# Kernel optimization log

Measured on AMD Instinct MI355X. Metric: run time of the kernel, lower is better.

## Reference

```python
import jax, jax.numpy as jnp
import numpy as np

B, T, D = 4, 512, 512
NB, NH, PF, K = 2, 8, 2, 4
INNER = PF * D          # 1024
DH = INNER // NH        # 128
NC = 1000
EPS = 1e-5


def _ln(x, s, b):
    mu = x.mean(-1, keepdims=True)
    var = x.var(-1, keepdims=True)
    return (x - mu) / jnp.sqrt(var + EPS) * s + b


def _causal_conv(x, k, b):
    # x: [B,T,C], depthwise kernel k: [C,K]
    kk = k.shape[-1]
    xp = jnp.pad(x, ((0, 0), (kk - 1, 0), (0, 0)))
    t = x.shape[1]
    y = sum(xp[:, j:j + t, :] * k[:, j] for j in range(kk))
    return y + b


def _mlstm_scan(q, k, v, ip, fp):
    # q,k,v: [B,T,NH,DH]; ip,fp: [B,T,NH]
    b, t, nh, dh = q.shape
    C0 = jnp.zeros((b, nh, dh, dh), q.dtype)
    n0 = jnp.zeros((b, nh, dh), q.dtype)
    m0 = jnp.zeros((b, nh), q.dtype)

    def step(carry, xs):
        C, n, m = carry
        qt, kt, vt, ipt, fpt = xs
        fl = jax.nn.log_sigmoid(fpt)
        m_new = jnp.maximum(fl + m, ipt)
        i = jnp.exp(ipt - m_new)
        f = jnp.exp(fl + m - m_new)
        C = f[..., None, None] * C + i[..., None, None] * (vt[..., :, None] * kt[..., None, :])
        n = f[..., None] * n + i[..., None] * kt
        denom = jnp.maximum(jnp.abs(jnp.einsum('bhd,bhd->bh', n, qt)), 1.0)
        h = jnp.einsum('bhij,bhj->bhi', C, qt) / denom[..., None]
        return (C, n, m_new), h

    tm = lambda a: jnp.swapaxes(a, 0, 1)  # time-major
    _, h = jax.lax.scan(step, (C0, n0, m0), (tm(q), tm(k), tm(v), tm(ip), tm(fp)))
    return jnp.swapaxes(h, 0, 1)  # [B,T,NH,DH]


def _block(x, ln_s, ln_b, w_up, b_up, conv_k, conv_b, w_q, w_k, w_v,
           w_ig, b_ig, w_fg, b_fg, hn_s, w_down, b_down):
    b, t, d = x.shape
    xn = _ln(x, ln_s, ln_b)
    up = xn @ w_up + b_up                       # [B,T,2*INNER]
    xu, z = up[..., :INNER], up[..., INNER:]
    xc = jax.nn.silu(_causal_conv(xu, conv_k, conv_b))
    q = (xc @ w_q).reshape(b, t, NH, DH)
    k = (xc @ w_k).reshape(b, t, NH, DH) * (DH ** -0.5)
    v = (xu @ w_v).reshape(b, t, NH, DH)
    ip = xc @ w_ig + b_ig                       # [B,T,NH]
    fp = xc @ w_fg + b_fg
    h = _mlstm_scan(q, k, v, ip, fp)            # [B,T,NH,DH]
    mu = h.mean(-1, keepdims=True)
    var = h.var(-1, keepdims=True)
    h = (h - mu) / jnp.sqrt(var + EPS) * hn_s   # per-head norm, hn_s: [NH,DH]
    h = h.reshape(b, t, INNER) * jax.nn.silu(z)
    return x + h @ w_down + b_down


def setup_inputs() -> dict:
    key = jax.random.key(0)
    ks = jax.random.split(key, 24)
    g = lambda i, sh, sc: jax.random.normal(ks[i], sh, jnp.float32) * sc
    inp = {
        'x': g(0, (B, T, D), 1.0),
        'cls_token': g(1, (1, 1, D), 0.02),
        'ln_s': jnp.ones((NB, D)), 'ln_b': jnp.zeros((NB, D)),
        'w_up': g(2, (NB, D, 2 * INNER), D ** -0.5), 'b_up': jnp.zeros((NB, 2 * INNER)),
        'conv_k': g(3, (NB, INNER, K), 0.3), 'conv_b': jnp.zeros((NB, INNER)),
        'w_q': g(4, (NB, INNER, INNER), INNER ** -0.5),
        'w_k': g(5, (NB, INNER, INNER), INNER ** -0.5),
        'w_v': g(6, (NB, INNER, INNER), INNER ** -0.5),
        'w_ig': g(7, (NB, INNER, NH), INNER ** -0.5), 'b_ig': jnp.zeros((NB, NH)),
        'w_fg': g(8, (NB, INNER, NH), INNER ** -0.5),
        'b_fg': jnp.full((NB, NH), 3.0),
        'hn_s': jnp.ones((NB, NH, DH)),
        'w_down': g(9, (NB, INNER, D), INNER ** -0.5), 'b_down': jnp.zeros((NB, D)),
        'fc_ln_s': jnp.ones((D,)), 'fc_ln_b': jnp.zeros((D,)),
        'fc_w': g(10, (D, NC), D ** -0.5), 'fc_b': jnp.zeros((NC,)),
    }
    return inp


def reference(x, cls_token, ln_s, ln_b, w_up, b_up, conv_k, conv_b, w_q, w_k, w_v,
              w_ig, b_ig, w_fg, b_fg, hn_s, w_down, b_down,
              fc_ln_s, fc_ln_b, fc_w, fc_b):
    b = x.shape[0]
    # append class token at the last position ('last')
    h = jnp.concatenate([x, jnp.broadcast_to(cls_token, (b, 1, x.shape[-1]))], axis=1)
    for i in range(NB):
        h = _block(h, ln_s[i], ln_b[i], w_up[i], b_up[i], conv_k[i], conv_b[i],
                   w_q[i], w_k[i], w_v[i], w_ig[i], b_ig[i], w_fg[i], b_fg[i],
                   hn_s[i], w_down[i], b_down[i])
    cls = h[:, -1, :]
    y = jax.nn.relu(_ln(cls, fc_ln_s, fc_ln_b)) @ fc_w + fc_b
    return y
```

## Files before the change

kernel.cpp:

```cpp
#include <hip/hip_runtime.h>

#define EPSV 1e-5f
constexpr int Bsz = 4, T0 = 512, Dm = 512, NHh = 8, KK = 4;
constexpr int TT = 513;
constexpr int IN = 1024, DHd = 128, NCc = 1000;
constexpr int ROWS = Bsz * TT;
constexpr int MPAD = 2176;
constexpr int NCH = 9;

constexpr size_t WT_UP = 0;
constexpr size_t WT_Q  = WT_UP + 2048 * 512;
constexpr size_t WT_K  = WT_Q + 1024 * 1024;
constexpr size_t WT_V  = WT_K + 1024 * 1024;
constexpr size_t WT_DN = WT_V + 1024 * 1024;
constexpr size_t WT_STRIDE = WT_DN + 512 * 1024;

typedef __attribute__((ext_vector_type(8))) short bf16x8;
typedef __attribute__((ext_vector_type(4))) float f32x4;
typedef __attribute__((ext_vector_type(4))) unsigned short ushort4v;
typedef __attribute__((ext_vector_type(8))) unsigned short ushort8v;
typedef unsigned short u16;

__device__ __forceinline__ float siluf(float x) { return x / (1.f + __expf(-x)); }
__device__ __forceinline__ u16 f2bf(float f) {
    unsigned int u = __float_as_uint(f);
    u = (u + 0x7FFFu + ((u >> 16) & 1u)) >> 16;
    return (u16)u;
}
__device__ __forceinline__ float bfu(u16 u) {
    return __uint_as_float(((unsigned int)u) << 16);
}
__device__ __forceinline__ void gload16(const u16* g, u16* l) {
    __builtin_amdgcn_global_load_lds(
        (const __attribute__((address_space(1))) void*)g,
        (__attribute__((address_space(3))) void*)l, 16, 0, 0);
}

template<bool CAT>
__global__ __launch_bounds__(256) void ln_kernel(const float* __restrict__ in,
                                                 const float* __restrict__ x,
                                                 const float* __restrict__ cls,
                                                 const float* __restrict__ s,
                                                 const float* __restrict__ bb,
                                                 float* __restrict__ hout,
                                                 u16* __restrict__ out16) {
    int row = blockIdx.x, tid = threadIdx.x;
    float x0, x1;
    if (CAT) {
        int b = row / TT, t = row - b * TT;
        const float* src = (t < T0) ? (x + ((size_t)(b * T0 + t)) * Dm) : cls;
        x0 = src[tid]; x1 = src[tid + 256];
        hout[(size_t)row * Dm + tid] = x0;
        hout[(size_t)row * Dm + tid + 256] = x1;
    } else {
        const float* r = in + (size_t)row * Dm;
        x0 = r[tid]; x1 = r[tid + 256];
    }
    __shared__ float s1[4], s2[4];
    float sum = x0 + x1, sq = x0 * x0 + x1 * x1;
#pragma unroll
    for (int o = 32; o > 0; o >>= 1) { sum += __shfl_xor(sum, o); sq += __shfl_xor(sq, o); }
    if ((tid & 63) == 0) { s1[tid >> 6] = sum; s2[tid >> 6] = sq; }
    __syncthreads();
    sum = s1[0] + s1[1] + s1[2] + s1[3];
    sq  = s2[0] + s2[1] + s2[2] + s2[3];
    float mu = sum / Dm, var = sq / Dm - mu * mu, inv = rsqrtf(var + EPSV);
    out16[(size_t)row * Dm + tid]       = f2bf((x0 - mu) * inv * s[tid] + bb[tid]);
    out16[(size_t)row * Dm + tid + 256] = f2bf((x1 - mu) * inv * s[tid + 256] + bb[tid + 256]);
}

__global__ __launch_bounds__(256) void w_transpose_kernel(const float* __restrict__ wup,
        const float* __restrict__ wq, const float* __restrict__ wk,
        const float* __restrict__ wv, const float* __restrict__ wdn,
        const float* __restrict__ wig, const float* __restrict__ wfg,
        u16* __restrict__ wt, float* __restrict__ gwt) {
    int y = blockIdx.y;
    if (y >= 10) {
        int blk = y - 10;
        int idx = blockIdx.x * 256 + threadIdx.x;
        if (idx < 16 * IN) {
            int k = idx & 1023;
            int g = (idx >> 10) & 15;
            const float* w = (g < 8) ? (wig + (size_t)blk * IN * NHh)
                                     : (wfg + (size_t)blk * IN * NHh);
            gwt[(size_t)blk * 16 * IN + idx] = w[k * NHh + (g & 7)];
        }
        return;
    }
    int blk = y / 5, sel = y - blk * 5;
    int Kd, N; const float* src; size_t doff;
    if (sel == 0)      { Kd = 512;  N = 2048; src = wup + (size_t)blk * 512 * 2048; doff = WT_UP; }
    else if (sel == 1) { Kd = 1024; N = 1024; src = wq  + (size_t)blk * 1024 * 1024; doff = WT_Q; }
    else if (sel == 2) { Kd = 1024; N = 1024; src = wk  + (size_t)blk * 1024 * 1024; doff = WT_K; }
    else if (sel == 3) { Kd = 1024; N = 1024; src = wv  + (size_t)blk * 1024 * 1024; doff = WT_V; }
    else               { Kd = 1024; N = 512;  src = wdn + (size_t)blk * 1024 * 512;  doff = WT_DN; }
    u16* dst = wt + (size_t)blk * WT_STRIDE + doff;
    int ntx = N >> 5;
    int ntiles = ntx * (Kd >> 5);
    int ti = blockIdx.x;
    if (ti >= ntiles) return;
    int tk = ti / ntx, tn = ti - tk * ntx;
    __shared__ u16 s[32][33];
    int tx = threadIdx.x & 31, ty = threadIdx.x >> 5;
#pragma unroll
    for (int i = 0; i < 4; i++) {
        int k = tk * 32 + ty + i * 8;
        s[ty + i * 8][tx] = f2bf(src[(size_t)k * N + tn * 32 + tx]);
    }
    __syncthreads();
#pragma unroll
    for (int i = 0; i < 4; i++) {
        int n = tn * 32 + ty + i * 8;
        dst[(size_t)n * Kd + tk * 32 + tx] = s[tx][ty + i * 8];
    }
}

template<int BM, int BN>
__device__ __forceinline__ void gemm_tile_body(const u16* __restrict__ A, int lda,
                                               const u16* __restrict__ Wt, int Kd,
                                               const float* __restrict__ bias,
                                               const float* __restrict__ resid, int ldr,
                                               float* __restrict__ Cout, int ldc,
                                               int M, float scale, int m0, int n0,
                                               u16 (*As)[BM][40], u16 (*Bs)[BN][40]) {
    constexpr int MT = BM / 32;
    constexpr int NT = BN / 32;
    constexpr int ANV = BM / 64;
    constexpr int BNV = BN / 64;
    int tid = threadIdx.x;
    int wave = tid >> 6, lane = tid & 63;
    int wm = (wave >> 1) * (BM / 2), wn = (wave & 1) * (BN / 2);
    int lrow = lane & 15, lquad = lane >> 4;

    f32x4 acc[MT][NT];
#pragma unroll
    for (int i = 0; i < MT; i++)
#pragma unroll
        for (int j = 0; j < NT; j++)
#pragma unroll
            for (int r = 0; r < 4; r++) acc[i][j][r] = 0.f;

    int am, ak, bn, bk;
    if (BM == 128) { am = tid >> 1; ak = (tid & 1) * 16; }
    else           { am = tid >> 2; ak = (tid & 3) * 8; }
    if (BN == 128) { bn = tid & 127; bk = (tid >> 7) * 16; }
    else           { bn = tid & 63;  bk = (tid >> 6) * 8; }
    int gm = m0 + am;
    const u16* arow = A + (size_t)(gm < M ? gm : 0) * lda + ak;
    bool avalid = gm < M;
    const u16* wrow = Wt + (size_t)(n0 + bn) * Kd + bk;

    ushort8v areg[ANV];
    ushort8v breg[BNV];

    auto load_tile = [&](int k0) {
        if (avalid) {
#pragma unroll
            for (int i = 0; i < ANV; i++) areg[i] = *(const ushort8v*)(arow + k0 + i * 8);
        } else {
#pragma unroll
            for (int i = 0; i < ANV; i++) areg[i] = (ushort8v){0,0,0,0,0,0,0,0};
        }
#pragma unroll
        for (int i = 0; i < BNV; i++) breg[i] = *(const ushort8v*)(wrow + k0 + i * 8);
    };
    auto store_tile = [&](int buf) {
#pragma unroll
        for (int i = 0; i < ANV; i++)
            *(ushort8v*)&As[buf][am][ak + i * 8] = areg[i];
#pragma unroll
        for (int i = 0; i < BNV; i++)
            *(ushort8v*)&Bs[buf][bn][bk + i * 8] = breg[i];
    };

    load_tile(0);
    store_tile(0);
    __syncthreads();

    int nk = Kd >> 5;
#pragma unroll 1
    for (int it = 0; it < nk; it++) {
        int cur = it & 1;
        bool more = (it + 1 < nk);
        if (more) load_tile((it + 1) << 5);
        bf16x8 afr[MT], bfr[NT];
#pragma unroll
        for (int mt = 0; mt < MT; mt++)
            afr[mt] = *(const bf16x8*)&As[cur][wm + mt * 16 + lrow][lquad * 8];
#pragma unroll
        for (int nt = 0; nt < NT; nt++)
            bfr[nt] = *(const bf16x8*)&Bs[cur][wn + nt * 16 + lrow][lquad * 8];
#pragma unroll
        for (int mt = 0; mt < MT; mt++)
#pragma unroll
            for (int nt = 0; nt < NT; nt++)
                acc[mt][nt] = __builtin_amdgcn_mfma_f32_16x16x32_bf16(
                    afr[mt], bfr[nt], acc[mt][nt], 0, 0, 0);
        if (more) store_tile(cur ^ 1);
        __syncthreads();
    }

#pragma unroll
    for (int mt = 0; mt < MT; mt++) {
#pragma unroll
        for (int r = 0; r < 4; r++) {
            int gmr = m0 + wm + mt * 16 + lquad * 4 + r;
            if (gmr >= M) continue;
#pragma unroll
            for (int nt = 0; nt < NT; nt++) {
                int gn = n0 + wn + nt * 16 + lrow;
                float v = acc[mt][nt][r] * scale;
                if (bias) v += bias[gn];
                if (resid) v += resid[(size_t)gmr * ldr + gn];
                Cout[(size_t)gmr * ldc + gn] = v;
            }
        }
    }
}

template<int BM, int BN>
__global__ __launch_bounds__(256, 2) void gemm_mfma_kernel(const u16* __restrict__ A, int lda,
                                                           const u16* __restrict__ Wt, int Kd,
                                                           const float* __restrict__ bias,
                                                           const float* __restrict__ resid, int ldr,
                                                           float* __restrict__ Cout, int ldc,
                                                           int M, float scale) {
    __shared__ __align__(16) u16 As[2][BM][40];
    __shared__ __align__(16) u16 Bs[2][BN][40];
    gemm_tile_body<BM, BN>(A, lda, Wt, Kd, bias, resid, ldr, Cout, ldc, M, scale,
                           blockIdx.y * BM, blockIdx.x * BN, As, Bs);
}

template<bool OUT16>
__device__ __forceinline__ void gemm128_body(const u16* __restrict__ A, int lda,
                                             const u16* __restrict__ Wt, int Kd,
                                             const float* __restrict__ bias,
                                             void* __restrict__ Cout, int ldc,
                                             int M, float scale, int m0, int n0,
                                             u16* As, u16* Bs) {
    int tid = threadIdx.x;
    int wave = tid >> 6, lane = tid & 63;
    int lrow = lane & 15, lquad = lane >> 4;
    int wm = (wave >> 1) * 64, wn = (wave & 1) * 64;

    const u16* ag0 = A + (size_t)(m0 + wave * 16 + (lane >> 2)) * lda + (lane & 3) * 8;
    const u16* ag1 = ag0 + (size_t)64 * lda;
    const u16* bg0 = Wt + (size_t)(n0 + wave * 16 + (lane >> 2)) * Kd + (lane & 3) * 8;
    const u16* bg1 = bg0 + (size_t)64 * Kd;

    auto stage = [&](int buf, int k0) {
        u16* a = As + buf * 4096 + wave * 512;
        u16* bb = Bs + buf * 4096 + wave * 512;
        gload16(ag0 + k0, a);
        gload16(ag1 + k0, a + 2048);
        gload16(bg0 + k0, bb);
        gload16(bg1 + k0, bb + 2048);
    };

    f32x4 acc[4][4];
#pragma unroll
    for (int i = 0; i < 4; i++)
#pragma unroll
        for (int j = 0; j < 4; j++)
#pragma unroll
            for (int r = 0; r < 4; r++) acc[i][j][r] = 0.f;

    int nk = Kd >> 5;
    stage(0, 0);
    __syncthreads();
#pragma unroll 1
    for (int it = 0; it < nk; it++) {
        int cur = it & 1;
        if (it + 1 < nk) stage(cur ^ 1, (it + 1) << 5);
        const u16* Ac = As + cur * 4096;
        const u16* Bc = Bs + cur * 4096;
        bf16x8 afr[4], bfr[4];
#pragma unroll
        for (int mt = 0; mt < 4; mt++)
            afr[mt] = *(const bf16x8*)&Ac[(wm + mt * 16 + lrow) * 32 + lquad * 8];
#pragma unroll
        for (int nt = 0; nt < 4; nt++)
            bfr[nt] = *(const bf16x8*)&Bc[(wn + nt * 16 + lrow) * 32 + lquad * 8];
#pragma unroll
        for (int mt = 0; mt < 4; mt++)
#pragma unroll
            for (int nt = 0; nt < 4; nt++)
                acc[mt][nt] = __builtin_amdgcn_mfma_f32_16x16x32_bf16(
                    afr[mt], bfr[nt], acc[mt][nt], 0, 0, 0);
        __syncthreads();
    }

#pragma unroll
    for (int mt = 0; mt < 4; mt++) {
#pragma unroll
        for (int r = 0; r < 4; r++) {
            int gmr = m0 + wm + mt * 16 + lquad * 4 + r;
            if (gmr >= M) continue;
#pragma unroll
            for (int nt = 0; nt < 4; nt++) {
                int gn = n0 + wn + nt * 16 + lrow;
                float v = acc[mt][nt][r] * scale;
                if (bias) v += bias[gn];
                if (OUT16) ((u16*)Cout)[(size_t)gmr * ldc + gn] = f2bf(v);
                else       ((float*)Cout)[(size_t)gmr * ldc + gn] = v;
            }
        }
    }
}

__global__ __launch_bounds__(256, 2) void up_gl_kernel(const u16* __restrict__ A,
        const u16* __restrict__ Wt, const float* __restrict__ bias, float* __restrict__ C) {
    __shared__ __align__(16) u16 As[2 * 4096];
    __shared__ __align__(16) u16 Bs[2 * 4096];
    gemm128_body<false>(A, Dm, Wt, Dm, bias, C, 2 * IN, ROWS, 1.f,
                        blockIdx.y * 128, blockIdx.x * 128, As, Bs);
}

__global__ __launch_bounds__(256, 2) void qkv_gl_kernel(const u16* __restrict__ xc16,
                                                        const u16* __restrict__ xu16,
                                                        const u16* __restrict__ wtblk,
                                                        u16* __restrict__ fq,
                                                        u16* __restrict__ fk,
                                                        u16* __restrict__ fv,
                                                        float kscale) {
    __shared__ __align__(16) u16 As[2 * 4096];
    __shared__ __align__(16) u16 Bs[2 * 4096];
    int sel = blockIdx.x >> 3, nx = blockIdx.x & 7;
    const u16* A = (sel == 2) ? xu16 : xc16;
    const u16* Wt = wtblk + ((sel == 0) ? WT_Q : (sel == 1) ? WT_K : WT_V);
    u16* C = (sel == 0) ? fq : (sel == 1) ? fk : fv;
    float scale = (sel == 1) ? kscale : 1.f;
    gemm128_body<true>(A, IN, Wt, IN, nullptr, C, IN, ROWS, scale,
                       blockIdx.y * 128, nx * 128, As, Bs);
}

__global__ __launch_bounds__(256) void convgates_kernel(const float* __restrict__ up,
        const float* __restrict__ ck, const float* __restrict__ cb,
        const float* __restrict__ wt, const float* __restrict__ big,
        const float* __restrict__ bfg,
        u16* __restrict__ xc16, u16* __restrict__ xu16,
        float* __restrict__ ip, float* __restrict__ fp) {
    int row = blockIdx.x, tid = threadIdx.x;
    int b = row / TT, t = row - b * TT;
    __shared__ float sx[IN];
    int c0 = tid * 4;
    float4 cur = *(const float4*)(up + (size_t)row * (2 * IN) + c0);
    float a0 = cb[c0 + 0] + cur.x * ck[(c0 + 0) * KK + 3];
    float a1 = cb[c0 + 1] + cur.y * ck[(c0 + 1) * KK + 3];
    float a2 = cb[c0 + 2] + cur.z * ck[(c0 + 2) * KK + 3];
    float a3 = cb[c0 + 3] + cur.w * ck[(c0 + 3) * KK + 3];
#pragma unroll
    for (int j = 0; j < KK - 1; j++) {
        int tt2 = t - (KK - 1) + j;
        if (tt2 >= 0) {
            float4 pv = *(const float4*)(up + ((size_t)(b * TT + tt2)) * (2 * IN) + c0);
            a0 += pv.x * ck[(c0 + 0) * KK + j];
            a1 += pv.y * ck[(c0 + 1) * KK + j];
            a2 += pv.z * ck[(c0 + 2) * KK + j];
            a3 += pv.w * ck[(c0 + 3) * KK + j];
        }
    }
    float s0 = siluf(a0), s1v = siluf(a1), s2v = siluf(a2), s3v = siluf(a3);
    *(float4*)&sx[c0] = make_float4(s0, s1v, s2v, s3v);
    ushort4v xc4 = {f2bf(s0), f2bf(s1v), f2bf(s2v), f2bf(s3v)};
    *(ushort4v*)&xc16[(size_t)row * IN + c0] = xc4;
    ushort4v xu4 = {f2bf(cur.x), f2bf(cur.y), f2bf(cur.z), f2bf(cur.w)};
    *(ushort4v*)&xu16[(size_t)row * IN + c0] = xu4;
    __syncthreads();

    int g = tid >> 4, l = tid & 15;
    const float* wrow = wt + g * IN;
    float acc = 0.f;
#pragma unroll
    for (int j = 0; j < 16; j++) {
        int k = j * 64 + l * 4;
        float4 w4 = *(const float4*)(wrow + k);
        float4 x4 = *(const float4*)&sx[k];
        acc += w4.x * x4.x + w4.y * x4.y + w4.z * x4.z + w4.w * x4.w;
    }
#pragma unroll
    for (int o = 8; o > 0; o >>= 1) acc += __shfl_down(acc, o, 16);
    if (l == 0) {
        if (g < 8) ip[(size_t)row * NHh + g] = acc + big[g];
        else       fp[(size_t)row * NHh + (g - 8)] = acc + bfg[g - 8];
    }
}

__global__ __launch_bounds__(256, 2) void chunk_state_kernel(const u16* __restrict__ kk,
        const u16* __restrict__ vv, const float* __restrict__ ip,
        const float* __restrict__ fp, float* __restrict__ gG, float* __restrict__ gM,
        float* __restrict__ gMb, float* __restrict__ gDec,
        u16* __restrict__ P16, float* __restrict__ nP) {
    int c = blockIdx.x, chain = blockIdx.y;
    int b = chain >> 3, h = chain & 7;
    int t0 = c * 64;
    int nvalid = min(64, TT - t0);
    __shared__ __align__(16) u16 sWv[128][72];
    __shared__ __align__(16) u16 sKt[128][72];
    __shared__ float sw[64];
    __shared__ float sGf[TT];
    __shared__ float sMbl[NCH];
    int tid = threadIdx.x;

    if (tid < 64) {
        constexpr int PER = 9;
        int lane = tid;
        int tbase = lane * PER;
        float lcs[PER], gi[PER];
        float csum = 0.f;
#pragma unroll
        for (int i = 0; i < PER; i++) {
            int t = tbase + i;
            float fpv = 0.f, ipv = 0.f;
            if (t < TT) {
                size_t gidx = (size_t)(b * TT + t) * NHh + h;
                fpv = fp[gidx]; ipv = ip[gidx];
            }
            float flv = (fpv >= 0.f) ? -log1pf(__expf(-fpv)) : (fpv - log1pf(__expf(fpv)));
            if (t >= TT) flv = 0.f;
            csum += flv;
            lcs[i] = csum;
            gi[i] = ipv;
        }
        float ps = csum;
#pragma unroll
        for (int o = 1; o < 64; o <<= 1) {
            float v = __shfl_up(ps, o);
            if (lane >= o) ps += v;
        }
        float Fexcl = ps - csum;
        float G[PER];
        float cmax = -1e30f;
#pragma unroll
        for (int i = 0; i < PER; i++) {
            int t = tbase + i;
            G[i] = (t < TT) ? (gi[i] - (Fexcl + lcs[i])) : -1e30f;
            cmax = fmaxf(cmax, G[i]);
            lcs[i] = cmax;
        }
        float pm = cmax;
#pragma unroll
        for (int o = 1; o < 64; o <<= 1) {
            float v = __shfl_up(pm, o);
            if (lane >= o) pm = fmaxf(pm, v);
        }
        float Me = __shfl_up(pm, 1);
        if (lane == 0) Me = -1e30f;
#pragma unroll
        for (int i = 0; i < PER; i++) {
            int t = tbase + i;
            if (t < TT) {
                float Mt = fmaxf(0.f, fmaxf(Me, lcs[i]));
                sGf[t] = G[i];
                if (c == 0) { gG[chain * TT + t] = G[i]; gM[chain * TT + t] = Mt; }
                if (((t & 63) == 63) || t == TT - 1) sMbl[t >> 6] = Mt;
            }
        }
    }
    __syncthreads();
    if (c == 0 && tid < NCH) {
        float Mbv = sMbl[tid];
        float Mbp = (tid == 0) ? 0.f : sMbl[tid - 1];
        gMb[chain * NCH + tid] = Mbv;
        gDec[chain * NCH + tid] = __expf(Mbp - Mbv);
    }
    if (tid < 64) {
        float Mb = sMbl[c];
        sw[tid] = (tid < nvalid) ? __expf(sGf[t0 + tid] - Mb) : 0.f;
    }
    __syncthreads();

    {
        int j = tid >> 2, d0 = (tid & 3) * 32;
        bool val = j < nvalid;
        float wj = sw[j];
        size_t gb = ((size_t)(b * TT + t0 + j)) * IN + h * DHd + d0;
        ushort8v z8 = {0,0,0,0,0,0,0,0};
#pragma unroll
        for (int i = 0; i < 4; i++) {
            ushort8v k8 = val ? *(const ushort8v*)(kk + gb + i * 8) : z8;
            ushort8v v8 = val ? *(const ushort8v*)(vv + gb + i * 8) : z8;
#pragma unroll
            for (int e = 0; e < 8; e++) {
                int dd = d0 + i * 8 + e;
                int jc = j ^ (((dd >> 5) & 3) << 4);
                sKt[dd][jc] = k8[e];
                sWv[dd][jc] = f2bf(bfu(v8[e]) * wj);
            }
        }
    }
    __syncthreads();

    int wave = tid >> 6, lane = tid & 63;
    int lrow = lane & 15, lquad = lane >> 4;
    int wm = (wave >> 1) * 64, wn = (wave & 1) * 64;
    f32x4 acc[4][4];
#pragma unroll
    for (int mt = 0; mt < 4; mt++)
#pragma unroll
        for (int nt = 0; nt < 4; nt++)
#pragma unroll
            for (int r = 0; r < 4; r++) acc[mt][nt][r] = 0.f;

#pragma unroll
    for (int ks = 0; ks < 2; ks++) {
        bf16x8 af[4], bfr[4];
#pragma unroll
        for (int mt = 0; mt < 4; mt++) {
            int r = wm + mt * 16 + lrow;
            int g = (ks * 4 + lquad) ^ (((r >> 5) & 3) << 1);
            af[mt] = *(const bf16x8*)&sWv[r][g * 8];
        }
#pragma unroll
        for (int nt = 0; nt < 4; nt++) {
            int r = wn + nt * 16 + lrow;
            int g = (ks * 4 + lquad) ^ (((r >> 5) & 3) << 1);
            bfr[nt] = *(const bf16x8*)&sKt[r][g * 8];
        }
#pragma unroll
        for (int mt = 0; mt < 4; mt++)
#pragma unroll
            for (int nt = 0; nt < 4; nt++)
                acc[mt][nt] = __builtin_amdgcn_mfma_f32_16x16x32_bf16(
                    af[mt], bfr[nt], acc[mt][nt], 0, 0, 0);
    }

    u16* Pbase = P16 + (((size_t)(c * 32 + chain)) << 14);
#pragma unroll
    for (int mt = 0; mt < 4; mt++)
#pragma unroll
        for (int r = 0; r < 4; r++) {
            int e = wm + mt * 16 + lquad * 4 + r;
#pragma unroll
            for (int nt = 0; nt < 4; nt++) {
                int d = wn + nt * 16 + lrow;
                Pbase[(size_t)e * 128 + d] = f2bf(acc[mt][nt][r]);
            }
        }

    {
        int d = tid >> 1, jh = (tid & 1) * 32;
        int swz = ((d >> 5) & 3) << 4;
        float an = 0.f;
#pragma unroll
        for (int j = 0; j < 32; j++) {
            int jj = jh + j;
            an += sw[jj] * bfu(sKt[d][jj ^ swz]);
        }
        an += __shfl_xor(an, 1);
        if ((tid & 1) == 0) nP[(size_t)(c * 32 + chain) * 128 + d] = an;
    }
}

__global__ __launch_bounds__(256) void chunk_combine_kernel(const u16* __restrict__ P16,
        u16* __restrict__ CB, float* __restrict__ nP, const float* __restrict__ gDec) {
    int chain = blockIdx.x >> 6;
    int seg = blockIdx.x & 63;
    int idx = seg * 256 + threadIdx.x;
    float run = 0.f;
    for (int c = 0; c < NCH; c++) {
        size_t a = (((size_t)(c * 32 + chain)) << 14) + idx;
        float tmp = bfu(P16[a]);
        CB[a] = f2bf(run);
        run = run * gDec[chain * NCH + c] + tmp;
    }
    if (seg == 0 && threadIdx.x < 128) {
        int d = threadIdx.x;
        float rn = 0.f;
        for (int c = 0; c < NCH; c++) {
            size_t a = (size_t)(c * 32 + chain) * 128 + d;
            float tmp = nP[a];
            nP[a] = rn;
            rn = rn * gDec[chain * NCH + c] + tmp;
        }
    }
}

__global__ __launch_bounds__(512, 2) void chunk_out_kernel(const u16* __restrict__ qq,
        const u16* __restrict__ kk, const u16* __restrict__ vv,
        const float* __restrict__ gG, const float* __restrict__ gM,
        const float* __restrict__ gMb, const u16* __restrict__ CB,
        const float* __restrict__ nP, const float* __restrict__ hn,
        const float* __restrict__ up, u16* __restrict__ out16) {
    int c = blockIdx.x, chain = blockIdx.y;
    int b = chain >> 3, h = chain & 7;
    int t0 = c * 64;
    int nvalid = min(64, TT - t0);
    __shared__ __align__(16) u16 smem[30720];
    __shared__ float sG[64], sM[64], sWr[64], sInv[64], sNb[128], sRS[2][64];
    u16* sQ  = smem;
    u16* sCB = smem + 8704;
    u16* sK  = smem + 8704;
    u16* sVt = smem;
    u16* sD  = smem + 26112;
    float* hv = (float*)smem;
    int tid = threadIdx.x;
    int wave = tid >> 6, lane = tid & 63;
    int lrow = lane & 15, lquad = lane >> 4;
    int mq = wave >> 1, nh = wave & 1;

    float Mbprev = (c > 0) ? gMb[chain * NCH + c - 1] : 0.f;
    if (tid < 64) {
        bool val = tid < nvalid;
        sG[tid] = val ? gG[chain * TT + t0 + tid] : -1e30f;
        float Mv = val ? gM[chain * TT + t0 + tid] : 1e30f;
        sM[tid] = Mv;
        sWr[tid] = val ? __expf(Mbprev - Mv) : 0.f;
    }
    if (tid >= 128 && tid < 256) sNb[tid - 128] = nP[(size_t)(c * 32 + chain) * 128 + (tid - 128)];

    ushort8v z8 = {0,0,0,0,0,0,0,0};
    {
        int lr = tid >> 3, c0 = (tid & 7) * 16;
        bool val = lr < nvalid;
        size_t gb = ((size_t)(b * TT + t0 + lr)) * IN + h * DHd + c0;
#pragma unroll
        for (int i = 0; i < 2; i++)
            *(ushort8v*)&sQ[lr * 136 + c0 + i * 8] =
                val ? *(const ushort8v*)(qq + gb + i * 8) : z8;
    }
    {
        const u16* CBbase = CB + (((size_t)(c * 32 + chain)) << 14);
        int e = tid >> 2, d0 = (tid & 3) * 32;
#pragma unroll
        for (int i = 0; i < 4; i++)
            *(ushort8v*)&sCB[e * 136 + d0 + i * 8] =
                *(const ushort8v*)(CBbase + (size_t)e * 128 + d0 + i * 8);
    }
    __syncthreads();

    f32x4 acc[4];
#pragma unroll
    for (int tt = 0; tt < 4; tt++)
#pragma unroll
        for (int r = 0; r < 4; r++) acc[tt][r] = 0.f;
#pragma unroll 1
    for (int ks = 0; ks < 4; ks++) {
        bf16x8 af = *(const bf16x8*)&sQ[(mq * 16 + lrow) * 136 + ks * 32 + lquad * 8];
#pragma unroll
        for (int tt = 0; tt < 4; tt++) {
            bf16x8 bf = *(const bf16x8*)&sCB[(nh * 64 + tt * 16 + lrow) * 136 + ks * 32 + lquad * 8];
            acc[tt] = __builtin_amdgcn_mfma_f32_16x16x32_bf16(af, bf, acc[tt], 0, 0, 0);
        }
    }
#pragma unroll
    for (int tt = 0; tt < 4; tt++)
#pragma unroll
        for (int r = 0; r < 4; r++) acc[tt][r] *= sWr[mq * 16 + lquad * 4 + r];
    __syncthreads();

    {
        int lr = tid >> 3, c0 = (tid & 7) * 16;
        bool val = lr < nvalid;
        size_t gb = ((size_t)(b * TT + t0 + lr)) * IN + h * DHd + c0;
#pragma unroll
        for (int i = 0; i < 2; i++)
            *(ushort8v*)&sK[lr * 136 + c0 + i * 8] =
                val ? *(const ushort8v*)(kk + gb + i * 8) : z8;
    }
    __syncthreads();

    {
        f32x4 accS[2];
#pragma unroll
        for (int tt = 0; tt < 2; tt++)
#pragma unroll
            for (int r = 0; r < 4; r++) accS[tt][r] = 0.f;
#pragma unroll 1
        for (int ks = 0; ks < 4; ks++) {
            bf16x8 af = *(const bf16x8*)&sQ[(mq * 16 + lrow) * 136 + ks * 32 + lquad * 8];
#pragma unroll
            for (int tt = 0; tt < 2; tt++) {
                bf16x8 bf = *(const bf16x8*)&sK[((nh * 2 + tt) * 16 + lrow) * 136 + ks * 32 + lquad * 8];
                accS[tt] = __builtin_amdgcn_mfma_f32_16x16x32_bf16(af, bf, accS[tt], 0, 0, 0);
            }
        }
        float rsum[4] = {0.f, 0.f, 0.f, 0.f};
#pragma unroll
        for (int tt = 0; tt < 2; tt++) {
            int j = (nh * 2 + tt) * 16 + lrow;
            float Gj = sG[j];
#pragma unroll
            for (int r = 0; r < 4; r++) {
                int t = mq * 16 + lquad * 4 + r;
                float w = (j <= t) ? __expf(Gj - sM[t]) : 0.f;
                float wD = accS[tt][r] * w;
                rsum[r] += wD;
                sD[t * 72 + j] = f2bf(wD);
            }
        }
#pragma unroll
        for (int r = 0; r < 4; r++) {
#pragma unroll
            for (int msk = 1; msk < 16; msk <<= 1) rsum[r] += __shfl_xor(rsum[r], msk);
        }
        if (lrow == 0) {
#pragma unroll
            for (int r = 0; r < 4; r++) sRS[nh][mq * 16 + lquad * 4 + r] = rsum[r];
        }
    }
    __syncthreads();

    if (tid < 64) {
        float qn = 0.f;
#pragma unroll 1
        for (int d4 = 0; d4 < 32; d4++) {
            ushort4v q4 = *(const ushort4v*)&sQ[tid * 136 + d4 * 4];
            float4 nb = *(const float4*)&sNb[d4 * 4];
            qn += bfu(q4.x) * nb.x + bfu(q4.y) * nb.y + bfu(q4.z) * nb.z + bfu(q4.w) * nb.w;
        }
        float den = sRS[0][tid] + sRS[1][tid] + sWr[tid] * qn;
        sInv[tid] = 1.f / fmaxf(fabsf(den), 1.f);
    }
    __syncthreads();

    {
        int e = tid & 127, tg = (tid >> 7) * 16;
#pragma unroll 1
        for (int i = 0; i < 16; i++) {
            int t = tg + i;
            sVt[e * 72 + t] = (t < nvalid) ? vv[((size_t)(b * TT + t0 + t)) * IN + h * DHd + e]
                                           : (u16)0;
        }
    }
    __syncthreads();

#pragma unroll 1
    for (int ks = 0; ks < 2; ks++) {
        bf16x8 af = *(const bf16x8*)&sD[(mq * 16 + lrow) * 72 + ks * 32 + lquad * 8];
#pragma unroll
        for (int tt = 0; tt < 4; tt++) {
            bf16x8 bf = *(const bf16x8*)&sVt[(nh * 64 + tt * 16 + lrow) * 72 + ks * 32 + lquad * 8];
            acc[tt] = __builtin_amdgcn_mfma_f32_16x16x32_bf16(af, bf, acc[tt], 0, 0, 0);
        }
    }

    __syncthreads();
#pragma unroll
    for (int tt = 0; tt < 4; tt++) {
#pragma unroll
        for (int r = 0; r < 4; r++) {
            int t = mq * 16 + lquad * 4 + r;
            int e = nh * 64 + tt * 16 + lrow;
            hv[t * 132 + e] = acc[tt][r] * sInv[t];
        }
    }
    __syncthreads();
    {
        int t = tid >> 3, s = tid & 7;
        float vals[16];
        float sum = 0.f, sq = 0.f;
#pragma unroll
        for (int i = 0; i < 16; i++) {
            float v = hv[t * 132 + s * 16 + i];
            vals[i] = v; sum += v; sq += v * v;
        }
#pragma unroll
        for (int m = 1; m < 8; m <<= 1) { sum += __shfl_xor(sum, m); sq += __shfl_xor(sq, m); }
        float mu = sum / DHd, var = sq / DHd - mu * mu, inv2 = rsqrtf(var + EPSV);
        if (t < nvalid) {
            size_t bt = (size_t)(b * TT + t0 + t);
            const float* zp = up + bt * (2 * IN) + IN + h * DHd + s * 16;
            u16* op = out16 + bt * IN + h * DHd + s * 16;
#pragma unroll
            for (int i = 0; i < 16; i++) {
                float hnv = hn[h * DHd + s * 16 + i];
                op[i] = f2bf((vals[i] - mu) * inv2 * hnv * siluf(zp[i]));
            }
        }
    }
}

__global__ __launch_bounds__(256) void fc_kernel(const float* __restrict__ hbuf,
                                                 const float* __restrict__ fcls,
                                                 const float* __restrict__ fclb,
                                                 const float* __restrict__ fw,
                                                 const float* __restrict__ fb,
                                                 float* __restrict__ out) {
    __shared__ float svc[Bsz][Dm];
    __shared__ float sred[4][256];
    int tid = threadIdx.x;
    int j0 = blockIdx.x * 64;
    {
        int r = tid >> 6, lane = tid & 63;
        const float* hrow = hbuf + ((size_t)r * TT + TT - 1) * Dm;
        float v[8];
        float sum = 0.f, sq = 0.f;
#pragma unroll
        for (int k = 0; k < 8; k++) {
            v[k] = hrow[lane + k * 64];
            sum += v[k]; sq += v[k] * v[k];
        }
#pragma unroll
        for (int o = 32; o > 0; o >>= 1) { sum += __shfl_xor(sum, o); sq += __shfl_xor(sq, o); }
        float mu = sum / Dm, var = sq / Dm - mu * mu, inv = rsqrtf(var + EPSV);
#pragma unroll
        for (int k = 0; k < 8; k++) {
            int e = lane + k * 64;
            svc[r][e] = fmaxf((v[k] - mu) * inv * fcls[e] + fclb[e], 0.f);
        }
    }
    __syncthreads();
    int j = j0 + (tid & 63);
    int chunk = tid >> 6;
    int kbase = chunk * 128;
    float a0 = 0.f, a1 = 0.f, a2 = 0.f, a3 = 0.f;
    if (j < NCc) {
        const float* fwp = fw + (size_t)kbase * NCc + j;
#pragma unroll 4
        for (int kk = 0; kk < 128; kk++) {
            float w = fwp[(size_t)kk * NCc];
            a0 += svc[0][kbase + kk] * w;
            a1 += svc[1][kbase + kk] * w;
            a2 += svc[2][kbase + kk] * w;
            a3 += svc[3][kbase + kk] * w;
        }
    }
    int jl = tid & 63;
    sred[chunk][jl * 4 + 0] = a0;
    sred[chunk][jl * 4 + 1] = a1;
    sred[chunk][jl * 4 + 2] = a2;
    sred[chunk][jl * 4 + 3] = a3;
    __syncthreads();
    if (tid < 64) {
        int jj = j0 + tid;
        if (jj < NCc) {
            float bias = fb[jj];
#pragma unroll
            for (int b = 0; b < Bsz; b++) {
                float v = sred[0][tid * 4 + b] + sred[1][tid * 4 + b]
                        + sred[2][tid * 4 + b] + sred[3][tid * 4 + b];
                out[b * NCc + jj] = v + bias;
            }
        }
    }
}

extern "C" void kernel_launch(void* const* d_in, const int* in_sizes, int n_in,
                              void* d_out, int out_size, void* d_ws, size_t ws_size,
                              hipStream_t stream) {
    const float* x      = (const float*)d_in[0];
    const float* cls    = (const float*)d_in[1];
    const float* ln_s   = (const float*)d_in[2];
    const float* ln_b   = (const float*)d_in[3];
    const float* w_up   = (const float*)d_in[4];
    const float* b_up   = (const float*)d_in[5];
    const float* conv_k = (const float*)d_in[6];
    const float* conv_b = (const float*)d_in[7];
    const float* w_q    = (const float*)d_in[8];
    const float* w_k    = (const float*)d_in[9];
    const float* w_v    = (const float*)d_in[10];
    const float* w_ig   = (const float*)d_in[11];
    const float* b_ig   = (const float*)d_in[12];
    const float* w_fg   = (const float*)d_in[13];
    const float* b_fg   = (const float*)d_in[14];
    const float* hn_s   = (const float*)d_in[15];
    const float* w_down = (const float*)d_in[16];
    const float* b_down = (const float*)d_in[17];
    const float* fcls   = (const float*)d_in[18];
    const float* fclb   = (const float*)d_in[19];
    const float* fc_w   = (const float*)d_in[20];
    const float* fc_b   = (const float*)d_in[21];
    float* out = (float*)d_out;

    float* ws = (float*)d_ws;
    size_t off = 0;
    float* f_h  = ws + off; off += (size_t)ROWS * Dm;
    float* f_up = ws + off; off += (size_t)ROWS * 2 * IN;
    float* f_ip = ws + off; off += (size_t)ROWS * NHh;
    float* f_fp = ws + off; off += (size_t)ROWS * NHh;
    float* g_G  = ws + off; off += 32 * TT;
    float* g_M  = ws + off; off += 32 * TT;
    float* g_Mb = ws + off; off += 32 * NCH;
    float* g_De = ws + off; off += 32 * NCH;
    float* g_nP = ws + off; off += (size_t)NCH * 32 * DHd;
    float* g_wt = ws + off; off += 2 * 16 * IN;
    u16* g_P16 = (u16*)(ws + off); off += ((size_t)NCH * 32 * DHd * DHd + 1) / 2;
    u16* g_CB  = (u16*)(ws + off); off += ((size_t)NCH * 32 * DHd * DHd + 1) / 2;
    u16* g_Wt  = (u16*)(ws + off); off += (2 * WT_STRIDE + 1) / 2;
    u16* f_xn16 = (u16*)(ws + off); off += ((size_t)MPAD * Dm) / 2;
    u16* f_xc16 = (u16*)(ws + off); off += ((size_t)MPAD * IN) / 2;
    u16* f_xu16 = (u16*)(ws + off); off += ((size_t)MPAD * IN) / 2;
    u16* f_xg16 = (u16*)(ws + off); off += ((size_t)ROWS * IN + 1) / 2;
    u16* f_q16  = (u16*)(ws + off); off += ((size_t)ROWS * IN + 1) / 2;
    u16* f_k16  = (u16*)(ws + off); off += ((size_t)ROWS * IN + 1) / 2;
    u16* f_v16  = (u16*)(ws + off); off += ((size_t)ROWS * IN + 1) / 2;

    const float kscale = 0.08838834764831845f;
    const int MB = (ROWS + 127) / 128;
    const int MB64 = (ROWS + 63) / 64;

    w_transpose_kernel<<<dim3(1024, 12), 256, 0, stream>>>(
        w_up, w_q, w_k, w_v, w_down, w_ig, w_fg, g_Wt, g_wt);

    for (int blk = 0; blk < 2; blk++) {
        const float* p_ln_s = ln_s + blk * Dm;
        const float* p_ln_b = ln_b + blk * Dm;
        const float* p_bup  = b_up + (size_t)blk * 2 * IN;
        const float* p_ck   = conv_k + (size_t)blk * IN * KK;
        const float* p_cb   = conv_b + (size_t)blk * IN;
        const float* p_big  = b_ig + (size_t)blk * NHh;
        const float* p_bfg  = b_fg + (size_t)blk * NHh;
        const float* p_hns  = hn_s + (size_t)blk * NHh * DHd;
        const float* p_bd   = b_down + (size_t)blk * Dm;
        const u16*   p_wt   = g_Wt + (size_t)blk * WT_STRIDE;

        if (blk == 0)
            ln_kernel<true><<<ROWS, 256, 0, stream>>>(nullptr, x, cls, p_ln_s, p_ln_b,
                                                      f_h, f_xn16);
        else
            ln_kernel<false><<<ROWS, 256, 0, stream>>>(f_h, nullptr, nullptr, p_ln_s, p_ln_b,
                                                       nullptr, f_xn16);

        up_gl_kernel<<<dim3(2 * IN / 128, MB), 256, 0, stream>>>(
            f_xn16, p_wt + WT_UP, p_bup, f_up);

        convgates_kernel<<<ROWS, 256, 0, stream>>>(
            f_up, p_ck, p_cb, g_wt + blk * 16 * IN, p_big, p_bfg,
            f_xc16, f_xu16, f_ip, f_fp);

        qkv_gl_kernel<<<dim3(24, MB), 256, 0, stream>>>(
            f_xc16, f_xu16, p_wt, f_q16, f_k16, f_v16, kscale);

        chunk_state_kernel<<<dim3(NCH, 32), 256, 0, stream>>>(
            f_k16, f_v16, f_ip, f_fp, g_G, g_M, g_Mb, g_De, g_P16, g_nP);
        chunk_combine_kernel<<<32 * 64, 256, 0, stream>>>(g_P16, g_CB, g_nP, g_De);
        chunk_out_kernel<<<dim3(NCH, 32), 512, 0, stream>>>(f_q16, f_k16, f_v16, g_G, g_M, g_Mb,
                                                            g_CB, g_nP, p_hns, f_up, f_xg16);

        gemm_mfma_kernel<64, 64><<<dim3(Dm / 64, MB64), 256, 0, stream>>>(
            f_xg16, IN, p_wt + WT_DN, IN, p_bd, f_h, Dm, f_h, Dm, ROWS, 1.f);
    }

    fc_kernel<<<(NCc + 63) / 64, 256, 0, stream>>>(f_h, fcls, fclb, fc_w, fc_b, out);
}
```

Measured before the change: 405.3 us.

## Add XCD-aware block swizzle to GEMMs and parallelize chunk q·n dot

Remaps GEMM workgroup IDs so consecutive tiles land on the same XCD, aiming for better L2 reuse of A and W tiles. In chunk_out_kernel, the per-row q·n normalizer dot product moves earlier and is split across all 512 threads with a shuffle reduction. This replaces a serial loop on 64 threads and lets one barrier be removed. The chunk_out launch bound rises to 4 blocks per CU, which caps registers and may cause spills. The swizzle assumes the workgroup count is divisible by 8; otherwise tiles could be remapped incorrectly.

```diff
diff --git a/kernel.cpp b/kernel.cpp
--- a/kernel.cpp
+++ b/kernel.cpp
@@ -115,6 +115,16 @@
     }
 }
 
+__device__ __forceinline__ void xcd_swz(int& bx, int& by) {
+    int nx = gridDim.x;
+    int nwg = nx * gridDim.y;
+    int bid = by * nx + bx;
+    int q = nwg >> 3;
+    int sw = (bid & 7) * q + (bid >> 3);
+    bx = sw % nx;
+    by = sw / nx;
+}
+
 template<int BM, int BN>
 __device__ __forceinline__ void gemm_tile_body(const u16* __restrict__ A, int lda,
                                                const u16* __restrict__ Wt, int Kd,
@@ -227,8 +237,10 @@
                                                            int M, float scale) {
     __shared__ __align__(16) u16 As[2][BM][40];
     __shared__ __align__(16) u16 Bs[2][BN][40];
+    int bx = blockIdx.x, by = blockIdx.y;
+    xcd_swz(bx, by);
     gemm_tile_body<BM, BN>(A, lda, Wt, Kd, bias, resid, ldr, Cout, ldc, M, scale,
-                           blockIdx.y * BM, blockIdx.x * BN, As, Bs);
+                           by * BM, bx * BN, As, Bs);
 }
 
 template<bool OUT16>
@@ -312,8 +324,10 @@
         const u16* __restrict__ Wt, const float* __restrict__ bias, float* __restrict__ C) {
     __shared__ __align__(16) u16 As[2 * 4096];
     __shared__ __align__(16) u16 Bs[2 * 4096];
+    int bx = blockIdx.x, by = blockIdx.y;
+    xcd_swz(bx, by);
     gemm128_body<false>(A, Dm, Wt, Dm, bias, C, 2 * IN, ROWS, 1.f,
-                        blockIdx.y * 128, blockIdx.x * 128, As, Bs);
+                        by * 128, bx * 128, As, Bs);
 }
 
 __global__ __launch_bounds__(256, 2) void qkv_gl_kernel(const u16* __restrict__ xc16,
@@ -325,13 +339,15 @@
                                                         float kscale) {
     __shared__ __align__(16) u16 As[2 * 4096];
     __shared__ __align__(16) u16 Bs[2 * 4096];
-    int sel = blockIdx.x >> 3, nx = blockIdx.x & 7;
+    int bx = blockIdx.x, by = blockIdx.y;
+    xcd_swz(bx, by);
+    int sel = bx >> 3, nx = bx & 7;
     const u16* A = (sel == 2) ? xu16 : xc16;
     const u16* Wt = wtblk + ((sel == 0) ? WT_Q : (sel == 1) ? WT_K : WT_V);
     u16* C = (sel == 0) ? fq : (sel == 1) ? fk : fv;
     float scale = (sel == 1) ? kscale : 1.f;
     gemm128_body<true>(A, IN, Wt, IN, nullptr, C, IN, ROWS, scale,
-                       blockIdx.y * 128, nx * 128, As, Bs);
+                       by * 128, nx * 128, As, Bs);
 }
 
 __global__ __launch_bounds__(256) void convgates_kernel(const float* __restrict__ up,
@@ -576,7 +592,7 @@
     }
 }
 
-__global__ __launch_bounds__(512, 2) void chunk_out_kernel(const u16* __restrict__ qq,
+__global__ __launch_bounds__(512, 4) void chunk_out_kernel(const u16* __restrict__ qq,
         const u16* __restrict__ kk, const u16* __restrict__ vv,
         const float* __restrict__ gG, const float* __restrict__ gM,
         const float* __restrict__ gMb, const u16* __restrict__ CB,
@@ -587,7 +603,7 @@
     int t0 = c * 64;
     int nvalid = min(64, TT - t0);
     __shared__ __align__(16) u16 smem[30720];
-    __shared__ float sG[64], sM[64], sWr[64], sInv[64], sNb[128], sRS[2][64];
+    __shared__ float sG[64], sM[64], sWr[64], sInv[64], sNb[128], sRS[2][64], sQn[64];
     u16* sQ  = smem;
     u16* sCB = smem + 8704;
     u16* sK  = smem + 8704;
@@ -629,6 +645,20 @@
     }
     __syncthreads();
 
+    {
+        int t = tid >> 3, s = tid & 7;
+        float qn = 0.f;
+#pragma unroll
+        for (int i = 0; i < 4; i++) {
+            ushort4v q4 = *(const ushort4v*)&sQ[t * 136 + s * 16 + i * 4];
+            float4 nb = *(const float4*)&sNb[s * 16 + i * 4];
+            qn += bfu(q4.x) * nb.x + bfu(q4.y) * nb.y + bfu(q4.z) * nb.z + bfu(q4.w) * nb.w;
+        }
+#pragma unroll
+        for (int m = 1; m < 8; m <<= 1) qn += __shfl_xor(qn, m);
+        if (s == 0) sQn[t] = qn;
+    }
+
     f32x4 acc[4];
 #pragma unroll
     for (int tt = 0; tt < 4; tt++)
@@ -702,18 +732,9 @@
     __syncthreads();
 
     if (tid < 64) {
-        float qn = 0.f;
-#pragma unroll 1
-        for (int d4 = 0; d4 < 32; d4++) {
-            ushort4v q4 = *(const ushort4v*)&sQ[tid * 136 + d4 * 4];
-            float4 nb = *(const float4*)&sNb[d4 * 4];
-            qn += bfu(q4.x) * nb.x + bfu(q4.y) * nb.y + bfu(q4.z) * nb.z + bfu(q4.w) * nb.w;
-        }
-        float den = sRS[0][tid] + sRS[1][tid] + sWr[tid] * qn;
+        float den = sRS[0][tid] + sRS[1][tid] + sWr[tid] * sQn[tid];
         sInv[tid] = 1.f / fmaxf(fabsf(den), 1.f);
     }
-    __syncthreads();
-
     {
         int e = tid & 127, tg = (tid >> 7) * 16;
 #pragma unroll 1
```

Result: no change. 402.0 us (-0.8%).
